# Optimization experiments

Measured on AMD Instinct MI355X. Metric: run time of the kernel, lower is better.

## Reference

```python
import jax, jax.numpy as jnp
import numpy as np

NUM_GROUP = 256   # npoint for FPS
GROUP_SIZE = 32   # k nearest neighbors per center


def setup_inputs() -> dict:
    key = jax.random.key(0)
    xyz = jax.random.normal(key, (32, 8192, 3), dtype=jnp.float32)  # (B,N,3)
    return {"xyz": xyz}


def _farthest_point_sample(xyz, npoint):
    # xyz: (B,N,3) -> indices (B,npoint). Deterministic start at index 0
    # (torch version uses randint; math of the iteration is identical).
    B, N, _ = xyz.shape
    init_dist = jnp.full((B, N), 1e10, dtype=xyz.dtype)
    init_far = jnp.zeros((B,), dtype=jnp.int32)

    def step(carry, _):
        distance, farthest = carry
        centroid = jnp.take_along_axis(xyz, farthest[:, None, None], axis=1)  # (B,1,3)
        d = jnp.sum((xyz - centroid) ** 2, axis=-1)           # (B,N)
        distance = jnp.minimum(distance, d)                    # masked update
        new_far = jnp.argmax(distance, axis=-1).astype(jnp.int32)
        return (distance, new_far), farthest

    _, cents = jax.lax.scan(step, (init_dist, init_far), None, length=npoint)
    return cents.T  # (B,npoint)


def _square_distance(src, dst):
    # src:(B,G,3), dst:(B,N,3) -> (B,G,N)
    return (jnp.sum(src ** 2, axis=-1)[:, :, None]
            - 2.0 * jnp.einsum('bgc,bnc->bgn', src, dst)
            + jnp.sum(dst ** 2, axis=-1)[:, None, :])


def reference(xyz):
    fps_idx = _farthest_point_sample(xyz, NUM_GROUP)                 # (B,G)
    center = jax.vmap(lambda p, i: p[i])(xyz, fps_idx)               # (B,G,3)
    dists = _square_distance(center, xyz)                            # (B,G,N)
    _, group_idx = jax.lax.top_k(-dists, GROUP_SIZE)                 # k smallest dists
    grouped = jax.vmap(lambda p, i: p[i])(xyz, group_idx)            # (B,G,K,3)
    group_feature = grouped.mean(axis=2)                             # (B,G,3)
    return (center, group_feature)
```

## Files before the change

### kernel.cpp

```cpp
#include <hip/hip_runtime.h>
#include <stdint.h>

typedef unsigned long long u64;
typedef unsigned int u32;

#define NB 32
#define NP 8192
#define NG 256
#define NK 32

__device__ __forceinline__ float dist3(float dx, float dy, float dz) {
    return __fadd_rn(__fadd_rn(__fmul_rn(dx, dx), __fmul_rn(dy, dy)), __fmul_rn(dz, dz));
}

#define DPP_STEP(v, ctrl, rmask) __builtin_amdgcn_update_dpp((int)(v), (int)(v), (ctrl), (rmask), 0xf, false)

__device__ __forceinline__ u32 wave_max_u32(u32 v) {
    u32 o;
    o = (u32)DPP_STEP(v, 0x111, 0xf); v = (o > v) ? o : v;
    o = (u32)DPP_STEP(v, 0x112, 0xf); v = (o > v) ? o : v;
    o = (u32)DPP_STEP(v, 0x114, 0xf); v = (o > v) ? o : v;
    o = (u32)DPP_STEP(v, 0x118, 0xf); v = (o > v) ? o : v;
    o = (u32)DPP_STEP(v, 0x142, 0xa); v = (o > v) ? o : v;
    o = (u32)DPP_STEP(v, 0x143, 0xc); v = (o > v) ? o : v;
    return (u32)__builtin_amdgcn_readlane((int)v, 63);
}

__device__ __forceinline__ u32 wave_min_u32(u32 v) {
    u32 o;
    o = (u32)DPP_STEP(v, 0x111, 0xf); v = (o < v) ? o : v;
    o = (u32)DPP_STEP(v, 0x112, 0xf); v = (o < v) ? o : v;
    o = (u32)DPP_STEP(v, 0x114, 0xf); v = (o < v) ? o : v;
    o = (u32)DPP_STEP(v, 0x118, 0xf); v = (o < v) ? o : v;
    o = (u32)DPP_STEP(v, 0x142, 0xa); v = (o < v) ? o : v;
    o = (u32)DPP_STEP(v, 0x143, 0xc); v = (o < v) ? o : v;
    return (u32)__builtin_amdgcn_readlane((int)v, 63);
}

__global__ __launch_bounds__(512) void fps_kernel(const float* __restrict__ xyz,
                                                  float* __restrict__ out)
{
    const int b = blockIdx.x;
    const int t = threadIdx.x;
    const int wid = t >> 6, lane = t & 63;

    __shared__ u64 wavekey[2][8];

    const float* base = xyz + (size_t)b * NP * 3;

    float px[16], py[16], pz[16], dist[16];
    {
        const float4* src = reinterpret_cast<const float4*>(base) + t * 12;
        float4 f[12];
        #pragma unroll
        for (int i = 0; i < 12; ++i) f[i] = src[i];
        float fl[48];
        #pragma unroll
        for (int i = 0; i < 12; ++i) {
            fl[4*i] = f[i].x; fl[4*i+1] = f[i].y; fl[4*i+2] = f[i].z; fl[4*i+3] = f[i].w;
        }
        #pragma unroll
        for (int j = 0; j < 16; ++j) {
            px[j] = fl[3*j]; py[j] = fl[3*j+1]; pz[j] = fl[3*j+2];
            dist[j] = 1e10f;
        }
    }

    float cx, cy, cz;
    {
        float4 f0 = *reinterpret_cast<const float4*>(base);
        cx = f0.x; cy = f0.y; cz = f0.z;
        if (t == 0) {
            float* o = out + (size_t)b * NG * 3;
            o[0] = cx; o[1] = cy; o[2] = cz;
        }
    }

    for (int g = 0; g < NG - 1; ++g) {
        float bestd = -1.0f;
        u32 bestj = 0;
        #pragma unroll
        for (int j = 0; j < 16; ++j) {
            float dx = __fsub_rn(px[j], cx);
            float dy = __fsub_rn(py[j], cy);
            float dz = __fsub_rn(pz[j], cz);
            float d  = dist3(dx, dy, dz);
            float dm = fminf(dist[j], d);
            dist[j] = dm;
            bool gt = dm > bestd;
            bestd = gt ? dm : bestd;
            bestj = gt ? (u32)j : bestj;
        }
        u32 hi = __float_as_uint(bestd);
        u32 lo = (u32)(NP - 1 - (t * 16 + (int)bestj));
        u32 mh = wave_max_u32(hi);
        u32 cl = (hi == mh) ? lo : 0u;
        u32 ml = wave_max_u32(cl);
        if (lane == 0) wavekey[g & 1][wid] = ((u64)mh << 32) | (u64)ml;
        __syncthreads();
        u64 wk = wavekey[g & 1][0];
        #pragma unroll
        for (int w = 1; w < 8; ++w) {
            u64 o = wavekey[g & 1][w];
            wk = (o > wk) ? o : wk;
        }
        const int widx = NP - 1 - (int)(u32)(wk & 0xFFFFFFFFull);
        const float* cp = base + (size_t)widx * 3;
        cx = cp[0]; cy = cp[1]; cz = cp[2];
        if (t == 0) {
            float* o = out + ((size_t)b * NG + g + 1) * 3;
            o[0] = cx; o[1] = cy; o[2] = cz;
        }
    }
}

__device__ __forceinline__ void build_top4(const float4* __restrict__ src,
                                           float cx, float cy, float cz, float s2,
                                           u64 L, bool useL, int lane,
                                           u64& t0, u64& t1, u64& t2, u64& t3)
{
    t0 = t1 = t2 = t3 = ~0ull;
    for (int q = 0; q < 32; ++q) {
        float4 f0 = src[q*3+0];
        float4 f1 = src[q*3+1];
        float4 f2 = src[q*3+2];
        float a[12] = {f0.x,f0.y,f0.z,f0.w, f1.x,f1.y,f1.z,f1.w, f2.x,f2.y,f2.z,f2.w};
        #pragma unroll
        for (int rr = 0; rr < 4; ++rr) {
            float nx = a[rr*3+0], ny = a[rr*3+1], nz = a[rr*3+2];
            float dotv = __fadd_rn(__fadd_rn(__fmul_rn(cx,nx), __fmul_rn(cy,ny)), __fmul_rn(cz,nz));
            float n2   = dist3(nx, ny, nz);
            float d    = __fadd_rn(__fsub_rn(s2, __fmul_rn(2.0f, dotv)), n2);
            u32 u  = __float_as_uint(d);
            u32 kk = u ^ (u32)(((int)u >> 31) | 0x80000000);
            int idx = lane * 128 + q * 4 + rr;
            u64 pk = ((u64)kk << 32) | (u64)(u32)idx;
            if (!useL || pk > L) {
                if (pk < t3) {
                    t3 = pk;
                    if (t3 < t2) { u64 tmp = t2; t2 = t3; t3 = tmp; }
                    if (t2 < t1) { u64 tmp = t1; t1 = t2; t2 = tmp; }
                    if (t1 < t0) { u64 tmp = t0; t0 = t1; t1 = tmp; }
                }
            }
        }
    }
}

__global__ __launch_bounds__(256) void knn_kernel(const float* __restrict__ xyz,
                                                  float* __restrict__ out)
{
    const int t    = threadIdx.x;
    const int lane = t & 63;
    const int wid  = t >> 6;
    const int task = blockIdx.x * 4 + wid;
    const int b    = task >> 8;
    const int g    = task & 255;

    const float* cptr = out + ((size_t)b * NG + g) * 3;
    const float cx = cptr[0], cy = cptr[1], cz = cptr[2];
    const float s2 = dist3(cx, cy, cz);

    const float4* src = reinterpret_cast<const float4*>(xyz + (size_t)b * NP * 3) + (size_t)lane * 96;

    u64 t0, t1, t2, t3;
    build_top4(src, cx, cy, cz, s2, 0ull, false, lane, t0, t1, t2, t3);
    int cnt = 4;
    u64 L = 0;
    u32 myWin = 0;

    for (int round = 0; round < NK; ++round) {
        if (cnt == 0) {
            build_top4(src, cx, cy, cz, s2, L, true, lane, t0, t1, t2, t3);
            cnt = 4;
        }
        u32 hi0 = (u32)(t0 >> 32), lo0 = (u32)(t0 & 0xFFFFFFFFull);
        u32 mh = wave_min_u32(hi0);
        u32 cl = (hi0 == mh) ? lo0 : 0xFFFFFFFFu;
        u32 ml = wave_min_u32(cl);
        u64 w  = ((u64)mh << 32) | (u64)ml;
        if (t0 == w) {
            t0 = t1; t1 = t2; t2 = t3; t3 = ~0ull;
            --cnt;
            L = w;
        }
        if (lane == round) myWin = ml;
    }

    float sx = 0.f, sy = 0.f, sz = 0.f;
    if (lane < NK) {
        const float* p = xyz + ((size_t)b * NP + myWin) * 3;
        sx = p[0]; sy = p[1]; sz = p[2];
    }
    #pragma unroll
    for (int m = 32; m >= 1; m >>= 1) {
        sx += __shfl_xor(sx, m, 64);
        sy += __shfl_xor(sy, m, 64);
        sz += __shfl_xor(sz, m, 64);
    }
    if (lane == 0) {
        float* o = out + (size_t)NB * NG * 3 + ((size_t)b * NG + g) * 3;
        const float inv = 1.0f / 32.0f;
        o[0] = sx * inv; o[1] = sy * inv; o[2] = sz * inv;
    }
}

extern "C" void kernel_launch(void* const* d_in, const int* in_sizes, int n_in,
                              void* d_out, int out_size, void* d_ws, size_t ws_size,
                              hipStream_t stream)
{
    const float* xyz = (const float*)d_in[0];
    float* out = (float*)d_out;

    hipLaunchKernelGGL(fps_kernel, dim3(NB), dim3(512), 0, stream, xyz, out);

    const int tasks  = NB * NG;
    const int blocks = tasks / 4;
    hipLaunchKernelGGL(knn_kernel, dim3(blocks), dim3(256), 0, stream, xyz, out);
}
```

Measured before the change: 369.4 us.

## Pack FPS distance math into float2 and stage KNN point loads through LDS

In the farthest-point-sampling kernel, each thread's 16 points are held as 8 two-wide float vectors, so the subtract, multiply and add steps can map to packed FP32 instructions. FP contraction is disabled to keep rounding identical to the reference. In the KNN kernel, each wave now loads point chunks cooperatively with coalesced float4 reads into double-buffered LDS, and points are interleaved across lanes instead of given to each lane as a contiguous strided slice. A top-4 refill now triggers a wave-wide rescan whenever any lane has run out, which may add redundant full scans in exchange for uniform control flow.

```diff
diff --git a/kernel.cpp b/kernel.cpp
--- a/kernel.cpp
+++ b/kernel.cpp
@@ -3,6 +3,7 @@
 
 typedef unsigned long long u64;
 typedef unsigned int u32;
+typedef float v2f __attribute__((ext_vector_type(2)));
 
 #define NB 32
 #define NP 8192
@@ -37,9 +38,10 @@
     return (u32)__builtin_amdgcn_readlane((int)v, 63);
 }
 
-__global__ __launch_bounds__(512) void fps_kernel(const float* __restrict__ xyz,
-                                                  float* __restrict__ out)
-{
+__global__ __launch_bounds__(512, 2) void fps_kernel(const float* __restrict__ xyz,
+                                                     float* __restrict__ out)
+{
+    #pragma clang fp contract(off)
     const int b = blockIdx.x;
     const int t = threadIdx.x;
     const int wid = t >> 6, lane = t & 63;
@@ -48,7 +50,7 @@
 
     const float* base = xyz + (size_t)b * NP * 3;
 
-    float px[16], py[16], pz[16], dist[16];
+    v2f px[8], py[8], pz[8], dist[8];
     {
         const float4* src = reinterpret_cast<const float4*>(base) + t * 12;
         float4 f[12];
@@ -60,9 +62,11 @@
             fl[4*i] = f[i].x; fl[4*i+1] = f[i].y; fl[4*i+2] = f[i].z; fl[4*i+3] = f[i].w;
         }
         #pragma unroll
-        for (int j = 0; j < 16; ++j) {
-            px[j] = fl[3*j]; py[j] = fl[3*j+1]; pz[j] = fl[3*j+2];
-            dist[j] = 1e10f;
+        for (int j = 0; j < 8; ++j) {
+            px[j] = (v2f){fl[6*j+0], fl[6*j+3]};
+            py[j] = (v2f){fl[6*j+1], fl[6*j+4]};
+            pz[j] = (v2f){fl[6*j+2], fl[6*j+5]};
+            dist[j] = (v2f){1e10f, 1e10f};
         }
     }
 
@@ -77,19 +81,30 @@
     }
 
     for (int g = 0; g < NG - 1; ++g) {
+        const v2f cvx = (v2f){cx, cx};
+        const v2f cvy = (v2f){cy, cy};
+        const v2f cvz = (v2f){cz, cz};
         float bestd = -1.0f;
         u32 bestj = 0;
         #pragma unroll
-        for (int j = 0; j < 16; ++j) {
-            float dx = __fsub_rn(px[j], cx);
-            float dy = __fsub_rn(py[j], cy);
-            float dz = __fsub_rn(pz[j], cz);
-            float d  = dist3(dx, dy, dz);
-            float dm = fminf(dist[j], d);
-            dist[j] = dm;
-            bool gt = dm > bestd;
-            bestd = gt ? dm : bestd;
-            bestj = gt ? (u32)j : bestj;
+        for (int j = 0; j < 8; ++j) {
+            v2f dx = px[j] - cvx;
+            v2f dy = py[j] - cvy;
+            v2f dz = pz[j] - cvz;
+            v2f qx = dx * dx;
+            v2f qy = dy * dy;
+            v2f qz = dz * dz;
+            v2f s  = (qx + qy) + qz;
+            float d0 = fminf(dist[j].x, s.x);
+            float d1 = fminf(dist[j].y, s.y);
+            dist[j].x = d0;
+            dist[j].y = d1;
+            bool g0 = d0 > bestd;
+            bestd = g0 ? d0 : bestd;
+            bestj = g0 ? (u32)(2*j) : bestj;
+            bool g1 = d1 > bestd;
+            bestd = g1 ? d1 : bestd;
+            bestj = g1 ? (u32)(2*j+1) : bestj;
         }
         u32 hi = __float_as_uint(bestd);
         u32 lo = (u32)(NP - 1 - (t * 16 + (int)bestj));
@@ -98,6 +113,7 @@
         u32 ml = wave_max_u32(cl);
         if (lane == 0) wavekey[g & 1][wid] = ((u64)mh << 32) | (u64)ml;
         __syncthreads();
+
         u64 wk = wavekey[g & 1][0];
         #pragma unroll
         for (int w = 1; w < 8; ++w) {
@@ -114,35 +130,56 @@
     }
 }
 
-__device__ __forceinline__ void build_top4(const float4* __restrict__ src,
-                                           float cx, float cy, float cz, float s2,
-                                           u64 L, bool useL, int lane,
-                                           u64& t0, u64& t1, u64& t2, u64& t3)
-{
+__device__ __forceinline__ void insert4(u64 pk, u64& t0, u64& t1, u64& t2, u64& t3) {
+    if (pk < t3) {
+        t3 = pk;
+        if (t3 < t2) { u64 tmp = t2; t2 = t3; t3 = tmp; }
+        if (t2 < t1) { u64 tmp = t1; t1 = t2; t2 = tmp; }
+        if (t1 < t0) { u64 tmp = t0; t0 = t1; t1 = tmp; }
+    }
+}
+
+__device__ __forceinline__ void scan_top4(const float4* __restrict__ gsrc,
+                                          float* __restrict__ buf0,
+                                          float* __restrict__ buf1,
+                                          float cx, float cy, float cz, float s2,
+                                          u64 L, bool useL, int lane,
+                                          u64& t0, u64& t1, u64& t2, u64& t3)
+{
+    #pragma clang fp contract(off)
     t0 = t1 = t2 = t3 = ~0ull;
-    for (int q = 0; q < 32; ++q) {
-        float4 f0 = src[q*3+0];
-        float4 f1 = src[q*3+1];
-        float4 f2 = src[q*3+2];
-        float a[12] = {f0.x,f0.y,f0.z,f0.w, f1.x,f1.y,f1.z,f1.w, f2.x,f2.y,f2.z,f2.w};
-        #pragma unroll
-        for (int rr = 0; rr < 4; ++rr) {
-            float nx = a[rr*3+0], ny = a[rr*3+1], nz = a[rr*3+2];
+
+    {
+        float4 a0 = gsrc[lane], a1 = gsrc[64 + lane], a2 = gsrc[128 + lane];
+        float4* w0 = reinterpret_cast<float4*>(buf0);
+        w0[lane] = a0; w0[64 + lane] = a1; w0[128 + lane] = a2;
+    }
+    float4 r0 = gsrc[192 + lane], r1 = gsrc[256 + lane], r2 = gsrc[320 + lane];
+
+    for (int c = 0; c < 32; ++c) {
+        float* cur = (c & 1) ? buf1 : buf0;
+        float* nxt = (c & 1) ? buf0 : buf1;
+        if (c < 31) {
+            float4* wn = reinterpret_cast<float4*>(nxt);
+            wn[lane] = r0; wn[64 + lane] = r1; wn[128 + lane] = r2;
+        }
+        if (c < 30) {
+            const float4* gn = gsrc + (size_t)(c + 2) * 192;
+            r0 = gn[lane]; r1 = gn[64 + lane]; r2 = gn[128 + lane];
+        }
+        #pragma unroll
+        for (int k = 0; k < 4; ++k) {
+            const int p = k * 64 + lane;
+            const float* q = cur + 3 * p;
+            float nx = q[0], ny = q[1], nz = q[2];
             float dotv = __fadd_rn(__fadd_rn(__fmul_rn(cx,nx), __fmul_rn(cy,ny)), __fmul_rn(cz,nz));
             float n2   = dist3(nx, ny, nz);
             float d    = __fadd_rn(__fsub_rn(s2, __fmul_rn(2.0f, dotv)), n2);
             u32 u  = __float_as_uint(d);
             u32 kk = u ^ (u32)(((int)u >> 31) | 0x80000000);
-            int idx = lane * 128 + q * 4 + rr;
+            int idx = c * 256 + p;
             u64 pk = ((u64)kk << 32) | (u64)(u32)idx;
-            if (!useL || pk > L) {
-                if (pk < t3) {
-                    t3 = pk;
-                    if (t3 < t2) { u64 tmp = t2; t2 = t3; t3 = tmp; }
-                    if (t2 < t1) { u64 tmp = t1; t1 = t2; t2 = tmp; }
-                    if (t1 < t0) { u64 tmp = t0; t0 = t1; t1 = tmp; }
-                }
-            }
+            if (!useL || pk > L) insert4(pk, t0, t1, t2, t3);
         }
     }
 }
@@ -150,6 +187,8 @@
 __global__ __launch_bounds__(256) void knn_kernel(const float* __restrict__ xyz,
                                                   float* __restrict__ out)
 {
+    __shared__ float ldsbuf[4][2][768];
+
     const int t    = threadIdx.x;
     const int lane = t & 63;
     const int wid  = t >> 6;
@@ -161,28 +200,31 @@
     const float cx = cptr[0], cy = cptr[1], cz = cptr[2];
     const float s2 = dist3(cx, cy, cz);
 
-    const float4* src = reinterpret_cast<const float4*>(xyz + (size_t)b * NP * 3) + (size_t)lane * 96;
+    const float4* gsrc = reinterpret_cast<const float4*>(xyz + (size_t)b * NP * 3);
+    float* buf0 = &ldsbuf[wid][0][0];
+    float* buf1 = &ldsbuf[wid][1][0];
 
     u64 t0, t1, t2, t3;
-    build_top4(src, cx, cy, cz, s2, 0ull, false, lane, t0, t1, t2, t3);
+    scan_top4(gsrc, buf0, buf1, cx, cy, cz, s2, 0ull, false, lane, t0, t1, t2, t3);
     int cnt = 4;
     u64 L = 0;
     u32 myWin = 0;
 
     for (int round = 0; round < NK; ++round) {
-        if (cnt == 0) {
-            build_top4(src, cx, cy, cz, s2, L, true, lane, t0, t1, t2, t3);
+        if (__ballot(cnt == 0) != 0ull) {
+            scan_top4(gsrc, buf0, buf1, cx, cy, cz, s2, L, L != 0ull, lane, t0, t1, t2, t3);
             cnt = 4;
         }
-        u32 hi0 = (u32)(t0 >> 32), lo0 = (u32)(t0 & 0xFFFFFFFFull);
+        u32 hi0 = (u32)(t0 >> 32);
+        u32 lo0 = (u32)(t0 & 0xFFFFFFFFull);
         u32 mh = wave_min_u32(hi0);
         u32 cl = (hi0 == mh) ? lo0 : 0xFFFFFFFFu;
         u32 ml = wave_min_u32(cl);
         u64 w  = ((u64)mh << 32) | (u64)ml;
         if (t0 == w) {
+            L = w;
             t0 = t1; t1 = t2; t2 = t3; t3 = ~0ull;
             --cnt;
-            L = w;
         }
         if (lane == round) myWin = ml;
     }
```

After: 378.3 us. 1.02x slower.

## Widen FPS block to 1024 threads and restructure KNN scan with coalesced interleaving

Applied to the files above, without the earlier changes.

The FPS kernel now uses 1024 threads with 8 points per thread instead of 512 with 16. The cross-wave max reduction is done with a DPP wave reduction over the 16 per-wave keys rather than a serial loop over shared memory. The KNN kernel interleaves points across lanes so loads are coalesced, and it keeps float distances and indices separately instead of packed 64-bit keys. It also rebuilds the per-lane top-4 for the whole wave whenever any lane's buffer empties, which can add extra full passes over the points.

```diff
diff --git a/kernel.cpp b/kernel.cpp
--- a/kernel.cpp
+++ b/kernel.cpp
@@ -37,33 +37,48 @@
     return (u32)__builtin_amdgcn_readlane((int)v, 63);
 }
 
-__global__ __launch_bounds__(512) void fps_kernel(const float* __restrict__ xyz,
-                                                  float* __restrict__ out)
+__device__ __forceinline__ float wave_min_f32(float v) {
+    float o;
+    o = __int_as_float(DPP_STEP(__float_as_int(v), 0x111, 0xf)); v = fminf(v, o);
+    o = __int_as_float(DPP_STEP(__float_as_int(v), 0x112, 0xf)); v = fminf(v, o);
+    o = __int_as_float(DPP_STEP(__float_as_int(v), 0x114, 0xf)); v = fminf(v, o);
+    o = __int_as_float(DPP_STEP(__float_as_int(v), 0x118, 0xf)); v = fminf(v, o);
+    o = __int_as_float(DPP_STEP(__float_as_int(v), 0x142, 0xa)); v = fminf(v, o);
+    o = __int_as_float(DPP_STEP(__float_as_int(v), 0x143, 0xc)); v = fminf(v, o);
+    return __int_as_float(__builtin_amdgcn_readlane(__float_as_int(v), 63));
+}
+
+__global__ __launch_bounds__(1024) void fps_kernel(const float* __restrict__ xyz,
+                                                   float* __restrict__ out)
 {
     const int b = blockIdx.x;
     const int t = threadIdx.x;
     const int wid = t >> 6, lane = t & 63;
 
-    __shared__ u64 wavekey[2][8];
+    __shared__ u64 wkey[2][16];
 
     const float* base = xyz + (size_t)b * NP * 3;
 
-    float px[16], py[16], pz[16], dist[16];
+    float px[8], py[8], pz[8], dist[8];
     {
-        const float4* src = reinterpret_cast<const float4*>(base) + t * 12;
-        float4 f[12];
-        #pragma unroll
-        for (int i = 0; i < 12; ++i) f[i] = src[i];
-        float fl[48];
-        #pragma unroll
-        for (int i = 0; i < 12; ++i) {
+        const float4* src = reinterpret_cast<const float4*>(base) + t * 6;
+        float4 f[6];
+        #pragma unroll
+        for (int i = 0; i < 6; ++i) f[i] = src[i];
+        float fl[24];
+        #pragma unroll
+        for (int i = 0; i < 6; ++i) {
             fl[4*i] = f[i].x; fl[4*i+1] = f[i].y; fl[4*i+2] = f[i].z; fl[4*i+3] = f[i].w;
         }
         #pragma unroll
-        for (int j = 0; j < 16; ++j) {
+        for (int j = 0; j < 8; ++j) {
             px[j] = fl[3*j]; py[j] = fl[3*j+1]; pz[j] = fl[3*j+2];
             dist[j] = 1e10f;
         }
+    }
+    #pragma unroll
+    for (int j = 0; j < 8; ++j) {
+        asm volatile("" : "+v"(px[j]), "+v"(py[j]), "+v"(pz[j]));
     }
 
     float cx, cy, cz;
@@ -80,7 +95,7 @@
         float bestd = -1.0f;
         u32 bestj = 0;
         #pragma unroll
-        for (int j = 0; j < 16; ++j) {
+        for (int j = 0; j < 8; ++j) {
             float dx = __fsub_rn(px[j], cx);
             float dy = __fsub_rn(py[j], cy);
             float dz = __fsub_rn(pz[j], cz);
@@ -92,19 +107,19 @@
             bestj = gt ? (u32)j : bestj;
         }
         u32 hi = __float_as_uint(bestd);
-        u32 lo = (u32)(NP - 1 - (t * 16 + (int)bestj));
+        u32 lo = (u32)(NP - 1 - (t * 8 + (int)bestj));
         u32 mh = wave_max_u32(hi);
         u32 cl = (hi == mh) ? lo : 0u;
         u32 ml = wave_max_u32(cl);
-        if (lane == 0) wavekey[g & 1][wid] = ((u64)mh << 32) | (u64)ml;
+        if (lane == 0) wkey[g & 1][wid] = ((u64)mh << 32) | (u64)ml;
         __syncthreads();
-        u64 wk = wavekey[g & 1][0];
-        #pragma unroll
-        for (int w = 1; w < 8; ++w) {
-            u64 o = wavekey[g & 1][w];
-            wk = (o > wk) ? o : wk;
-        }
-        const int widx = NP - 1 - (int)(u32)(wk & 0xFFFFFFFFull);
+
+        u64 k = wkey[g & 1][lane & 15];
+        u32 khi = (u32)(k >> 32), klo = (u32)(k & 0xFFFFFFFFull);
+        u32 mh2 = wave_max_u32(khi);
+        u32 cl2 = (khi == mh2) ? klo : 0u;
+        u32 ml2 = wave_max_u32(cl2);
+        const int widx = NP - 1 - (int)ml2;
         const float* cp = base + (size_t)widx * 3;
         cx = cp[0]; cy = cp[1]; cz = cp[2];
         if (t == 0) {
@@ -114,38 +129,25 @@
     }
 }
 
-__device__ __forceinline__ void build_top4(const float4* __restrict__ src,
-                                           float cx, float cy, float cz, float s2,
-                                           u64 L, bool useL, int lane,
-                                           u64& t0, u64& t1, u64& t2, u64& t3)
-{
-    t0 = t1 = t2 = t3 = ~0ull;
-    for (int q = 0; q < 32; ++q) {
-        float4 f0 = src[q*3+0];
-        float4 f1 = src[q*3+1];
-        float4 f2 = src[q*3+2];
-        float a[12] = {f0.x,f0.y,f0.z,f0.w, f1.x,f1.y,f1.z,f1.w, f2.x,f2.y,f2.z,f2.w};
-        #pragma unroll
-        for (int rr = 0; rr < 4; ++rr) {
-            float nx = a[rr*3+0], ny = a[rr*3+1], nz = a[rr*3+2];
-            float dotv = __fadd_rn(__fadd_rn(__fmul_rn(cx,nx), __fmul_rn(cy,ny)), __fmul_rn(cz,nz));
-            float n2   = dist3(nx, ny, nz);
-            float d    = __fadd_rn(__fsub_rn(s2, __fmul_rn(2.0f, dotv)), n2);
-            u32 u  = __float_as_uint(d);
-            u32 kk = u ^ (u32)(((int)u >> 31) | 0x80000000);
-            int idx = lane * 128 + q * 4 + rr;
-            u64 pk = ((u64)kk << 32) | (u64)(u32)idx;
-            if (!useL || pk > L) {
-                if (pk < t3) {
-                    t3 = pk;
-                    if (t3 < t2) { u64 tmp = t2; t2 = t3; t3 = tmp; }
-                    if (t2 < t1) { u64 tmp = t1; t1 = t2; t2 = tmp; }
-                    if (t1 < t0) { u64 tmp = t0; t0 = t1; t1 = tmp; }
-                }
-            }
-        }
-    }
-}
+__device__ __forceinline__ float3 ld3(const float* p) {
+    return *reinterpret_cast<const float3*>(p);
+}
+
+#define INSERT_PAIR(D, I) { \
+    if ((D) < td3) { \
+        td3 = (D); ti3 = (I); \
+        if (td3 < td2) { float tf = td2; td2 = td3; td3 = tf; u32 tu = ti2; ti2 = ti3; ti3 = tu; } \
+        if (td2 < td1) { float tf = td1; td1 = td2; td2 = tf; u32 tu = ti1; ti1 = ti2; ti2 = tu; } \
+        if (td1 < td0) { float tf = td0; td0 = td1; td1 = tf; u32 tu = ti0; ti0 = ti1; ti1 = tu; } \
+    } }
+
+#define KDIST(P, DVAR) \
+    float DVAR; { \
+        float nx = (P).x, ny = (P).y, nz = (P).z; \
+        float dotv = __fadd_rn(__fadd_rn(__fmul_rn(cx,nx), __fmul_rn(cy,ny)), __fmul_rn(cz,nz)); \
+        float n2   = dist3(nx, ny, nz); \
+        DVAR = __fadd_rn(__fsub_rn(s2, __fmul_rn(2.0f, dotv)), n2); \
+    }
 
 __global__ __launch_bounds__(256) void knn_kernel(const float* __restrict__ xyz,
                                                   float* __restrict__ out)
@@ -161,30 +163,67 @@
     const float cx = cptr[0], cy = cptr[1], cz = cptr[2];
     const float s2 = dist3(cx, cy, cz);
 
-    const float4* src = reinterpret_cast<const float4*>(xyz + (size_t)b * NP * 3) + (size_t)lane * 96;
-
-    u64 t0, t1, t2, t3;
-    build_top4(src, cx, cy, cz, s2, 0ull, false, lane, t0, t1, t2, t3);
+    const float* pts = xyz + (size_t)b * NP * 3;
+    const float* lp  = pts + lane * 3;
+
+    const float INF = __builtin_inff();
+    float td0, td1, td2, td3;
+    u32   ti0, ti1, ti2, ti3;
+    td0 = td1 = td2 = td3 = INF;
+    ti0 = ti1 = ti2 = ti3 = 0;
+
+    #pragma unroll 1
+    for (int c = 0; c < 32; ++c) {
+        const float* q = lp + (size_t)c * 768;
+        float3 p0 = ld3(q);
+        float3 p1 = ld3(q + 192);
+        float3 p2 = ld3(q + 384);
+        float3 p3 = ld3(q + 576);
+        const u32 ib = (u32)(c * 256 + lane);
+        KDIST(p0, d0) INSERT_PAIR(d0, ib)
+        KDIST(p1, d1) INSERT_PAIR(d1, ib + 64)
+        KDIST(p2, d2) INSERT_PAIR(d2, ib + 128)
+        KDIST(p3, d3) INSERT_PAIR(d3, ib + 192)
+    }
+
     int cnt = 4;
-    u64 L = 0;
+    float Ld = -INF;
+    u32   Li = 0;
     u32 myWin = 0;
-
-    for (int round = 0; round < NK; ++round) {
-        if (cnt == 0) {
-            build_top4(src, cx, cy, cz, s2, L, true, lane, t0, t1, t2, t3);
-            cnt = 4;
-        }
-        u32 hi0 = (u32)(t0 >> 32), lo0 = (u32)(t0 & 0xFFFFFFFFull);
-        u32 mh = wave_min_u32(hi0);
-        u32 cl = (hi0 == mh) ? lo0 : 0xFFFFFFFFu;
-        u32 ml = wave_min_u32(cl);
-        u64 w  = ((u64)mh << 32) | (u64)ml;
-        if (t0 == w) {
-            t0 = t1; t1 = t2; t2 = t3; t3 = ~0ull;
-            --cnt;
-            L = w;
-        }
-        if (lane == round) myWin = ml;
+    int round = 0;
+
+    for (;;) {
+        for (; round < NK; ++round) {
+            if (__ballot(cnt == 0) != 0ull) break;
+            float md = wave_min_f32(td0);
+            u32 ci = (td0 == md) ? ti0 : 0xFFFFFFFFu;
+            u32 mi = wave_min_u32(ci);
+            if (td0 == md && ti0 == mi) {
+                Ld = md; Li = mi;
+                td0 = td1; td1 = td2; td2 = td3; td3 = INF;
+                ti0 = ti1; ti1 = ti2; ti2 = ti3;
+                --cnt;
+            }
+            if (lane == round) myWin = mi;
+        }
+        if (round >= NK) break;
+
+        td0 = td1 = td2 = td3 = INF;
+        ti0 = ti1 = ti2 = ti3 = 0;
+        #pragma unroll 1
+        for (int c = 0; c < 32; ++c) {
+            const float* q = lp + (size_t)c * 768;
+            float3 p0 = ld3(q);
+            float3 p1 = ld3(q + 192);
+            float3 p2 = ld3(q + 384);
+            float3 p3 = ld3(q + 576);
+            const u32 ib = (u32)(c * 256 + lane);
+            KDIST(p0, d0) if (d0 > Ld || (d0 == Ld && ib       > Li)) INSERT_PAIR(d0, ib)
+            KDIST(p1, d1) if (d1 > Ld || (d1 == Ld && ib + 64  > Li)) INSERT_PAIR(d1, ib + 64)
+            KDIST(p2, d2) if (d2 > Ld || (d2 == Ld && ib + 128 > Li)) INSERT_PAIR(d2, ib + 128)
+            KDIST(p3, d3) if (d3 > Ld || (d3 == Ld && ib + 192 > Li)) INSERT_PAIR(d3, ib + 192)
+        }
+        cnt = 4;
     }
 
     float sx = 0.f, sy = 0.f, sz = 0.f;
@@ -212,7 +251,7 @@
     const float* xyz = (const float*)d_in[0];
     float* out = (float*)d_out;
 
-    hipLaunchKernelGGL(fps_kernel, dim3(NB), dim3(512), 0, stream, xyz, out);
+    hipLaunchKernelGGL(fps_kernel, dim3(NB), dim3(1024), 0, stream, xyz, out);
 
     const int tasks  = NB * NG;
     const int blocks = tasks / 4;
```

Result: slower. 401.2 us (+8.6%).
